# Kernel tuning notes

Measured on AMD Instinct MI355X. Metric: run time of the kernel, lower is better.

The kernel has to match this reference:

```python
import jax, jax.numpy as jnp
import numpy as np
import math

N, E, IN, C, H, ED, B = 50000, 800000, 64, 32, 4, 1, 64
HC = H * C
EPS = 1e-5


def setup_inputs() -> dict:
    key = jax.random.key(0)
    ks = jax.random.split(key, 16)
    def lin(k, fan_in, fan_out):
        s = 1.0 / math.sqrt(fan_in)
        return jax.random.normal(k, (fan_in, fan_out), jnp.float32) * s
    inp = {
        "x": jax.random.normal(ks[0], (N, IN), jnp.float32),
        "edge_index": jax.random.randint(ks[1], (2, E), 0, N, jnp.int64),
        "edge_attr": jax.random.normal(ks[2], (E, ED), jnp.float32),
        "batch_index": jnp.sort(jax.random.randint(ks[3], (N,), 0, B, jnp.int64)),
        # TransformerConv params
        "Wq": lin(ks[4], IN, HC), "bq": jnp.zeros((HC,), jnp.float32),
        "Wk": lin(ks[5], IN, HC), "bk": jnp.zeros((HC,), jnp.float32),
        "Wv": lin(ks[6], IN, HC), "bv": jnp.zeros((HC,), jnp.float32),
        "We": lin(ks[7], ED, HC), "be": jnp.zeros((HC,), jnp.float32),
        "Wskip": lin(ks[8], IN, HC), "bskip": jnp.zeros((HC,), jnp.float32),
        "Wbeta": lin(ks[9], 3 * HC, 1),
        # post linear: H*C -> C
        "Wlin": lin(ks[10], HC, C), "blin": jnp.zeros((C,), jnp.float32),
        # GraphNorm params
        "gn_weight": jnp.ones((C,), jnp.float32),
        "gn_bias": jnp.zeros((C,), jnp.float32),
        "gn_mean_scale": jnp.ones((C,), jnp.float32),
    }
    return inp


def reference(x, edge_index, edge_attr, batch_index, Wq, bq, Wk, bk, Wv, bv,
              We, be, Wskip, bskip, Wbeta, Wlin, blin,
              gn_weight, gn_bias, gn_mean_scale):
    src, dst = edge_index[0], edge_index[1]
    # dense projections [N, H, C]
    q = (x @ Wq + bq).reshape(N, H, C)
    k = (x @ Wk + bk).reshape(N, H, C)
    v = (x @ Wv + bv).reshape(N, H, C)
    e = (edge_attr @ We + be).reshape(E, H, C)
    # per-edge attention logits [E, H]
    k_e = k[src] + e
    alpha = jnp.einsum('ehc,ehc->eh', q[dst], k_e) / math.sqrt(C)
    # segment softmax over incoming edges of each dst node
    m = jax.ops.segment_max(alpha, dst, num_segments=N)  # [N, H]
    a = jnp.exp(alpha - m[dst])
    denom = jax.ops.segment_sum(a, dst, num_segments=N)  # [N, H]
    a = a / jnp.maximum(denom, 1e-16)[dst]
    # (dropout p=0.3 on attention is a no-op in eval mode)
    msg = (v[src] + e) * a[:, :, None]                    # [E, H, C]
    out = jax.ops.segment_sum(msg, dst, num_segments=N).reshape(N, HC)
    # beta-gated skip connection
    x_r = x @ Wskip + bskip                               # [N, HC]
    beta = jax.nn.sigmoid(jnp.concatenate([out, x_r, out - x_r], -1) @ Wbeta)
    out = beta * x_r + (1.0 - beta) * out
    # linear + relu
    h = jax.nn.relu(out @ Wlin + blin)                    # [N, C]
    # GraphNorm over per-graph segments
    ones = jnp.ones((N, 1), h.dtype)
    cnt = jax.ops.segment_sum(ones, batch_index, num_segments=B)  # [B, 1]
    cnt = jnp.maximum(cnt, 1.0)
    mean = jax.ops.segment_sum(h, batch_index, num_segments=B) / cnt
    centered = h - mean[batch_index] * gn_mean_scale
    var = jax.ops.segment_sum(centered * centered, batch_index, num_segments=B) / cnt
    std = jnp.sqrt(var + EPS)
    return gn_weight * centered / std[batch_index] + gn_bias
```

## Files before the change

### kernel.cpp

```cpp
#include <hip/hip_runtime.h>
#include <math.h>

static constexpr int kN  = 50000;
static constexpr int kE  = 800000;
static constexpr int kC  = 32;
static constexpr int kH  = 4;
static constexpr int kHC = 128;
static constexpr int kB  = 64;
static constexpr int kNB = (kN + 255) / 256;
static constexpr int kMB = (kN + 127) / 128;

typedef __attribute__((ext_vector_type(8))) short bf16x8;
typedef __attribute__((ext_vector_type(4))) float f32x4;

__device__ __forceinline__ unsigned short f2bf(float f) {
    unsigned u = __float_as_uint(f);
    unsigned r = (u + 0x7FFFu + ((u >> 16) & 1u)) >> 16;
    return (unsigned short)r;
}
__device__ __forceinline__ float blo(unsigned u) { return __uint_as_float(u << 16); }
__device__ __forceinline__ float bhi(unsigned u) { return __uint_as_float(u & 0xFFFF0000u); }

__global__ __launch_bounds__(256) void hist_packw_kernel(
    const int* __restrict__ ei, int* __restrict__ deg,
    const float* __restrict__ Wq, const float* __restrict__ Wk,
    const float* __restrict__ Wv, const float* __restrict__ Wskip,
    uint4* __restrict__ wtf)
{
    if (blockIdx.x < 16) {
        int tid = blockIdx.x * 256 + threadIdx.x;
        int f = tid >> 6, l = tid & 63;
        int m = f >> 4, c = (f >> 1) & 7, kk = f & 1;
        int col = c * 16 + (l & 15);
        int k0  = kk * 32 + (l >> 4) * 8;
        const float* Wm = (m == 0) ? Wq : (m == 1) ? Wk : (m == 2) ? Wv : Wskip;
        unsigned p[4];
#pragma unroll
        for (int j = 0; j < 4; ++j) {
            unsigned lo = f2bf(Wm[(k0 + 2 * j) * kHC + col]);
            unsigned hi = f2bf(Wm[(k0 + 2 * j + 1) * kHC + col]);
            p[j] = lo | (hi << 16);
        }
        wtf[f * 64 + l] = make_uint4(p[0], p[1], p[2], p[3]);
        return;
    }
    int i = (blockIdx.x - 16) * 256 + threadIdx.x;
    if (i < kE) atomicAdd(&deg[ei[kE + i]], 1);
}

__global__ __launch_bounds__(256) void proj_scanA_kernel(
    const float4* __restrict__ x4,
    const float* __restrict__ bq, const float* __restrict__ bk,
    const float* __restrict__ bv, const float* __restrict__ bskip,
    const uint4* __restrict__ wtf,
    unsigned short* __restrict__ qxb, unsigned short* __restrict__ kvb,
    const int* __restrict__ deg, int* __restrict__ bsum)
{
    __shared__ unsigned stg[2][32 * 128];
    if (blockIdx.x >= kMB) {
        int bid = blockIdx.x - kMB;
        int i = bid * 256 + threadIdx.x;
        int v = (i < kN) ? deg[i] : 0;
#pragma unroll
        for (int s = 1; s < 64; s <<= 1) v += __shfl_xor(v, s);
        if ((threadIdx.x & 63) == 0) stg[0][threadIdx.x >> 6] = (unsigned)v;
        __syncthreads();
        if (threadIdx.x == 0)
            bsum[bid] = (int)(stg[0][0] + stg[0][1] + stg[0][2] + stg[0][3]);
        return;
    }
    const int t = threadIdx.x;
    const int w = t >> 6;
    const int l = t & 63;
    const int l15 = l & 15, l16 = l >> 4;
    const int n0 = blockIdx.x * 128;

    bf16x8 bf[8][2];
#pragma unroll
    for (int c = 0; c < 8; ++c)
#pragma unroll
        for (int kk = 0; kk < 2; ++kk)
            bf[c][kk] = __builtin_bit_cast(bf16x8, wtf[(unsigned)((w * 16 + c * 2 + kk) * 64 + l)]);

    const float* Bm = (w == 0) ? bq : (w == 1) ? bk : (w == 2) ? bv : bskip;
    float bias[8];
#pragma unroll
    for (int c = 0; c < 8; ++c) bias[c] = Bm[c * 16 + l15];

    const int bufid = (w == 0 || w == 3) ? 0 : 1;
    const int add4  = (w >= 2) ? 4 : 0;

    for (int rt = 0; rt < 4; ++rt) {
        const int r0 = n0 + rt * 32 + l15;
        const int r1 = r0 + 16;
        f32x4 acc[2][8];
#pragma unroll
        for (int r = 0; r < 2; ++r)
#pragma unroll
            for (int c = 0; c < 8; ++c)
                acc[r][c] = (f32x4){bias[c], bias[c], bias[c], bias[c]};
#pragma unroll
        for (int kk = 0; kk < 2; ++kk) {
            float4 xa0 = make_float4(0.f,0.f,0.f,0.f), xb0 = xa0, xa1 = xa0, xb1 = xa0;
            if (r0 < kN) {
                xa0 = x4[(size_t)r0 * 16 + kk * 8 + l16 * 2];
                xb0 = x4[(size_t)r0 * 16 + kk * 8 + l16 * 2 + 1];
            }
            if (r1 < kN) {
                xa1 = x4[(size_t)r1 * 16 + kk * 8 + l16 * 2];
                xb1 = x4[(size_t)r1 * 16 + kk * 8 + l16 * 2 + 1];
            }
            uint4 u0 = make_uint4(
                f2bf(xa0.x) | ((unsigned)f2bf(xa0.y) << 16),
                f2bf(xa0.z) | ((unsigned)f2bf(xa0.w) << 16),
                f2bf(xb0.x) | ((unsigned)f2bf(xb0.y) << 16),
                f2bf(xb0.z) | ((unsigned)f2bf(xb0.w) << 16));
            uint4 u1 = make_uint4(
                f2bf(xa1.x) | ((unsigned)f2bf(xa1.y) << 16),
                f2bf(xa1.z) | ((unsigned)f2bf(xa1.w) << 16),
                f2bf(xb1.x) | ((unsigned)f2bf(xb1.y) << 16),
                f2bf(xb1.z) | ((unsigned)f2bf(xb1.w) << 16));
            bf16x8 a0 = __builtin_bit_cast(bf16x8, u0);
            bf16x8 a1 = __builtin_bit_cast(bf16x8, u1);
#pragma unroll
            for (int c = 0; c < 8; ++c) {
                acc[0][c] = __builtin_amdgcn_mfma_f32_16x16x32_bf16(a0, bf[c][kk], acc[0][c], 0, 0, 0);
                acc[1][c] = __builtin_amdgcn_mfma_f32_16x16x32_bf16(a1, bf[c][kk], acc[1][c], 0, 0, 0);
            }
        }
#pragma unroll
        for (int r = 0; r < 2; ++r) {
#pragma unroll
            for (int j = 0; j < 4; ++j) {
                int nn = r * 16 + l16 * 4 + j;
#pragma unroll
                for (int c = 0; c < 8; ++c) {
                    float v0 = acc[r][c][j];
                    float v1 = __shfl_xor(v0, 1);
                    if ((l & 1) == 0) {
                        int jcol = c * 16 + l15;
                        int gpos = ((jcol >> 2) << 3) | (jcol & 3);
                        stg[bufid][nn * 128 + ((gpos + add4) >> 1)] =
                            f2bf(v0) | ((unsigned)f2bf(v1) << 16);
                    }
                }
            }
        }
        __syncthreads();
#pragma unroll
        for (int i = 0; i < 8; ++i) {
            int idx = i * 256 + t;
            int buf = idx >> 10;
            int rem = idx & 1023;
            int nn  = rem >> 5;
            int q4  = rem & 31;
            int node = n0 + rt * 32 + nn;
            if (node < kN)
                ((uint4*)(buf ? kvb : qxb))[(size_t)node * 32 + q4] =
                    *(const uint4*)&stg[buf][nn * 128 + q4 * 4];
        }
        __syncthreads();
    }
}

__global__ __launch_bounds__(256) void scanC2_kernel(
    const int* __restrict__ deg, const int* __restrict__ bsum,
    int* __restrict__ rowptr, int* __restrict__ cursor)
{
    __shared__ int bsh[256];
    __shared__ int sh[256];
    const int t = threadIdx.x, i = blockIdx.x * 256 + t;
    int bv = (t < kNB) ? bsum[t] : 0;
    bsh[t] = bv; __syncthreads();
    for (int off = 1; off < 256; off <<= 1) {
        int u = (t >= off) ? bsh[t - off] : 0;
        __syncthreads();
        bsh[t] += u;
        __syncthreads();
    }
    const int bofs = (blockIdx.x == 0) ? 0 : bsh[blockIdx.x - 1];
    if (blockIdx.x == 0 && t == 0) rowptr[kN] = bsh[kNB - 1];
    int v = (i < kN) ? deg[i] : 0;
    sh[t] = v; __syncthreads();
    for (int off = 1; off < 256; off <<= 1) {
        int u = (t >= off) ? sh[t - off] : 0;
        __syncthreads();
        sh[t] += u;
        __syncthreads();
    }
    if (i < kN) {
        int ex = sh[t] - v + bofs;
        rowptr[i] = ex;
        cursor[i] = ex;
    }
}

__global__ __launch_bounds__(256) void scatter_kernel(
    const int* __restrict__ ei, const float* __restrict__ ea,
    int* __restrict__ cursor, unsigned* __restrict__ csr)
{
    int i = blockIdx.x * 256 + threadIdx.x;
    if (i >= kE) return;
    int dst = ei[kE + i];
    int slot = atomicAdd(&cursor[dst], 1);
    csr[slot] = (unsigned)ei[i] | ((unsigned)f2bf(ea[i]) << 16);
}

__global__ __launch_bounds__(512) void node_attn_kernel(
    const int* __restrict__ rowptr, const unsigned* __restrict__ csr,
    const unsigned short* __restrict__ qxb, const unsigned short* __restrict__ kvb,
    const float* __restrict__ We, const float* __restrict__ be,
    const float* __restrict__ Wbeta, const float* __restrict__ Wlin,
    const float* __restrict__ blin, float* __restrict__ hbuf)
{
    __shared__ float wlS[kHC * kC];
    __shared__ float wbS[3 * kHC];
    __shared__ float oshS[8][kHC];
    const int t = threadIdx.x, wv = t >> 6, lane = t & 63;
    for (int i = t; i < kHC * kC; i += 512) wlS[i] = Wlin[i];
    for (int i = t; i < 3 * kHC; i += 512) wbS[i] = Wbeta[i];
    __syncthreads();

    const int node = blockIdx.x * 8 + wv;
    const int half = lane >> 5;
    const int sl   = lane & 31;
    const int ch   = sl * 4;
    const float4 we4 = *(const float4*)&We[ch];
    const float4 be4 = *(const float4*)&be[ch];
    const float4 wbA = *(const float4*)&wbS[ch];
    const float4 wbB = *(const float4*)&wbS[kHC + ch];
    const float4 wbC = *(const float4*)&wbS[2 * kHC + ch];
    const float blc = blin[sl];
    const float A2 = 0.17677669529663687f * 1.44269504088896341f;

    const uint4 qx = *((const uint4*)(qxb + (size_t)node * 256) + sl);
    const float q0 = blo(qx.x), q1 = bhi(qx.x), q2v = blo(qx.y), q3 = bhi(qx.y);
    const float xr0 = blo(qx.z), xr1 = bhi(qx.z), xr2 = blo(qx.w), xr3 = bhi(qx.w);
    float qw = q0 * we4.x + q1 * we4.y + q2v * we4.z + q3 * we4.w;
    float qe = q0 * be4.x + q1 * be4.y + q2v * be4.z + q3 * be4.w;
    qw += __shfl_xor(qw, 1); qe += __shfl_xor(qe, 1);
    qw += __shfl_xor(qw, 2); qe += __shfl_xor(qe, 2);
    qw += __shfl_xor(qw, 4); qe += __shfl_xor(qe, 4);
    const float qwA = qw * A2, qbA = qe * A2;

    float ss = 0.f, swa = 0.f;
    float ax0 = 0.f, ax1 = 0.f, ax2 = 0.f, ax3 = 0.f;
    const int beg = rowptr[node], end = rowptr[node + 1];
    int e = beg;
    for (; e + 3 < end; e += 4) {
        unsigned cA = csr[e + half];
        unsigned cB = csr[e + 2 + half];
        float aA = bhi(cA), aB = bhi(cB);
        const uint4 uA = *((const uint4*)(kvb + (size_t)(cA & 0xFFFFu) * 256) + sl);
        const uint4 uB = *((const uint4*)(kvb + (size_t)(cB & 0xFFFFu) * 256) + sl);
        float pA = fmaf(q3, bhi(uA.y), fmaf(q2v, blo(uA.y), fmaf(q1, bhi(uA.x), q0 * blo(uA.x))));
        float pB = fmaf(q3, bhi(uB.y), fmaf(q2v, blo(uB.y), fmaf(q1, bhi(uB.x), q0 * blo(uB.x))));
        pA += __shfl_xor(pA, 1); pB += __shfl_xor(pB, 1);
        pA += __shfl_xor(pA, 2); pB += __shfl_xor(pB, 2);
        pA += __shfl_xor(pA, 4); pB += __shfl_xor(pB, 4);
        float eA = __builtin_amdgcn_exp2f(fmaf(pA, A2, fmaf(aA, qwA, qbA)));
        float eB = __builtin_amdgcn_exp2f(fmaf(pB, A2, fmaf(aB, qwA, qbA)));
        ss  += eA + eB;
        swa = fmaf(eA, aA, fmaf(eB, aB, swa));
        ax0 = fmaf(eA, blo(uA.z), fmaf(eB, blo(uB.z), ax0));
        ax1 = fmaf(eA, bhi(uA.z), fmaf(eB, bhi(uB.z), ax1));
        ax2 = fmaf(eA, blo(uA.w), fmaf(eB, blo(uB.w), ax2));
        ax3 = fmaf(eA, bhi(uA.w), fmaf(eB, bhi(uB.w), ax3));
    }
    for (; e < end; e += 2) {
        int idx = e + half;
        bool valid = idx < end;
        unsigned cA = csr[valid ? idx : end - 1];
        float aA = bhi(cA);
        const uint4 uA = *((const uint4*)(kvb + (size_t)(cA & 0xFFFFu) * 256) + sl);
        float pA = fmaf(q3, bhi(uA.y), fmaf(q2v, blo(uA.y), fmaf(q1, bhi(uA.x), q0 * blo(uA.x))));
        pA += __shfl_xor(pA, 1);
        pA += __shfl_xor(pA, 2);
        pA += __shfl_xor(pA, 4);
        float eA = valid ? __builtin_amdgcn_exp2f(fmaf(pA, A2, fmaf(aA, qwA, qbA))) : 0.f;
        ss  += eA;
        swa = fmaf(eA, aA, swa);
        ax0 = fmaf(eA, blo(uA.z), ax0);
        ax1 = fmaf(eA, bhi(uA.z), ax1);
        ax2 = fmaf(eA, blo(uA.w), ax2);
        ax3 = fmaf(eA, bhi(uA.w), ax3);
    }
    ss  += __shfl_xor(ss , 32);
    swa += __shfl_xor(swa, 32);
    ax0 += __shfl_xor(ax0, 32);
    ax1 += __shfl_xor(ax1, 32);
    ax2 += __shfl_xor(ax2, 32);
    ax3 += __shfl_xor(ax3, 32);

    float rcp = 1.f / fmaxf(ss, 1e-16f);
    float v0 = fmaf(swa, we4.x, fmaf(ss, be4.x, ax0)) * rcp;
    float v1 = fmaf(swa, we4.y, fmaf(ss, be4.y, ax1)) * rcp;
    float v2 = fmaf(swa, we4.z, fmaf(ss, be4.z, ax2)) * rcp;
    float v3 = fmaf(swa, we4.w, fmaf(ss, be4.w, ax3)) * rcp;
    float part = wbA.x * v0 + wbA.y * v1 + wbA.z * v2 + wbA.w * v3
               + wbB.x * xr0 + wbB.y * xr1 + wbB.z * xr2 + wbB.w * xr3
               + wbC.x * (v0 - xr0) + wbC.y * (v1 - xr1)
               + wbC.z * (v2 - xr2) + wbC.w * (v3 - xr3);
    part += __shfl_xor(part, 1);
    part += __shfl_xor(part, 2);
    part += __shfl_xor(part, 4);
    part += __shfl_xor(part, 8);
    part += __shfl_xor(part, 16);
    float beta = 1.f / (1.f + __expf(-part));
    float o0 = beta * xr0 + (1.f - beta) * v0;
    float o1 = beta * xr1 + (1.f - beta) * v1;
    float o2 = beta * xr2 + (1.f - beta) * v2;
    float o3 = beta * xr3 + (1.f - beta) * v3;
    if (half == 0) *(float4*)&oshS[wv][ch] = make_float4(o0, o1, o2, o3);
    __builtin_amdgcn_wave_barrier();
    float hp = 0.f;
#pragma unroll
    for (int jj = 0; jj < 64; ++jj) {
        int j = half * 64 + jj;
        hp = fmaf(oshS[wv][j], wlS[j * kC + sl], hp);
    }
    hp += __shfl_xor(hp, 32);
    if (lane < 32) hbuf[(size_t)node * kC + sl] = fmaxf(hp + blc, 0.f);
}

__global__ __launch_bounds__(256) void gn_reduce_kernel(
    const float* __restrict__ hbuf, const int* __restrict__ batch,
    const float* __restrict__ gms, float* __restrict__ stats)
{
    const int g = blockIdx.x;
    const int t = threadIdx.x;
    __shared__ int se[2];
    __shared__ float s1[8][kC], s2[8][kC];
    if (t < 2) {
        int target = g + t;
        int lo = 0, hi = kN;
        while (lo < hi) { int mid = (lo + hi) >> 1; if (batch[mid] < target) lo = mid + 1; else hi = mid; }
        se[t] = lo;
    }
    __syncthreads();
    int start = se[0], end = se[1];
    float cnt = fmaxf((float)(end - start), 1.f);
    int c = t & 31, r = t >> 5;
    float a = 0.f, b = 0.f;
    for (int n = start + r; n < end; n += 8) {
        float v = hbuf[(size_t)n * kC + c];
        a += v; b = fmaf(v, v, b);
    }
    s1[r][c] = a; s2[r][c] = b;
    __syncthreads();
    if (t < kC) {
        float sa = 0.f, sb = 0.f;
#pragma unroll
        for (int i = 0; i < 8; ++i) { sa += s1[i][t]; sb += s2[i][t]; }
        float mean = sa / cnt;
        float ms   = mean * gms[t];
        float var  = sb / cnt - 2.f * ms * mean + ms * ms;
        stats[g * 64 + t]      = ms;
        stats[g * 64 + 32 + t] = rsqrtf(var + 1e-5f);
    }
}

__global__ __launch_bounds__(256) void gn_apply_kernel(
    const float* __restrict__ hbuf, const int* __restrict__ batch,
    const float* __restrict__ stats,
    const float* __restrict__ gw, const float* __restrict__ gb,
    float* __restrict__ out)
{
    int idx = blockIdx.x * 256 + threadIdx.x;
    if (idx >= kN * kC) return;
    int n = idx >> 5, c = idx & 31;
    int g = batch[n];
    float ms   = stats[g * 64 + c];
    float rstd = stats[g * 64 + 32 + c];
    float v = hbuf[idx];
    out[idx] = fmaf(gw[c] * (v - ms), rstd, gb[c]);
}

extern "C" void kernel_launch(void* const* d_in, const int* in_sizes, int n_in,
                              void* d_out, int out_size, void* d_ws, size_t ws_size,
                              hipStream_t stream) {
    (void)in_sizes; (void)n_in; (void)out_size; (void)ws_size;
    const float* x     = (const float*)d_in[0];
    const int*   ei    = (const int*)d_in[1];
    const float* ea    = (const float*)d_in[2];
    const int*   batch = (const int*)d_in[3];
    const float* Wq    = (const float*)d_in[4];
    const float* bq    = (const float*)d_in[5];
    const float* Wk    = (const float*)d_in[6];
    const float* bk    = (const float*)d_in[7];
    const float* Wv    = (const float*)d_in[8];
    const float* bv    = (const float*)d_in[9];
    const float* We    = (const float*)d_in[10];
    const float* be    = (const float*)d_in[11];
    const float* Wskip = (const float*)d_in[12];
    const float* bskip = (const float*)d_in[13];
    const float* Wbeta = (const float*)d_in[14];
    const float* Wlin  = (const float*)d_in[15];
    const float* blin  = (const float*)d_in[16];
    const float* gw    = (const float*)d_in[17];
    const float* gb    = (const float*)d_in[18];
    const float* gms   = (const float*)d_in[19];
    float* out = (float*)d_out;

    char* ws = (char*)d_ws;
    unsigned* csr = (unsigned*)ws;        ws += (size_t)kE * 4;
    unsigned short* qxb = (unsigned short*)ws; ws += (size_t)kN * 256 * 2;
    unsigned short* kvb = (unsigned short*)ws; ws += (size_t)kN * 256 * 2;
    float* hbuf   = (float*)ws;           ws += (size_t)kN * kC * 4;
    int*   deg    = (int*)ws;             ws += (size_t)kN * 4;
    int*   cursor = (int*)ws;             ws += (size_t)kN * 4;
    int*   rowptr = (int*)ws;             ws += (size_t)(kN + 1) * 4;
    int*   bsum   = (int*)ws;             ws += (size_t)kNB * 4;
    float* stats  = (float*)ws;           ws += (size_t)kB * 64 * 4;
    uint4* wtf    = (uint4*)ws;           ws += (size_t)64 * 64 * 16;

    hipMemsetAsync(deg, 0, (size_t)kN * 4, stream);

    hist_packw_kernel<<<16 + (kE + 255) / 256, 256, 0, stream>>>(
        ei, deg, Wq, Wk, Wv, Wskip, wtf);
    proj_scanA_kernel<<<kMB + kNB, 256, 0, stream>>>(
        (const float4*)x, bq, bk, bv, bskip, wtf, qxb, kvb, deg, bsum);
    scanC2_kernel<<<kNB, 256, 0, stream>>>(deg, bsum, rowptr, cursor);
    scatter_kernel<<<(kE + 255) / 256, 256, 0, stream>>>(ei, ea, cursor, csr);
    node_attn_kernel<<<kN / 8, 512, 0, stream>>>(
        rowptr, csr, qxb, kvb, We, be, Wbeta, Wlin, blin, hbuf);
    gn_reduce_kernel<<<kB, 256, 0, stream>>>(hbuf, batch, gms, stats);
    gn_apply_kernel<<<(kN * kC + 255) / 256, 256, 0, stream>>>(
        hbuf, batch, stats, gw, gb, out);
}
```

Measured before the change: 238.7 us.

## Fuse GraphNorm reduce and apply; drop LDS staging in projection stores

The GraphNorm statistics and normalization passes are merged into one kernel with 512 threads per graph segment. Each block computes its segment's mean and rstd, keeps them in shared memory, and then normalizes the same rows, which removes a launch and the global stats buffer. Separately, the projection kernel now writes packed bf16 results straight to global memory instead of staging them in 32KB of LDS and copying out with uint4 stores. This drops two barriers per tile and frees LDS for occupancy, at the cost of scattered 4-byte writes from half the lanes. The fused GN kernel uses only 64 blocks, so its second pass over hbuf may be less parallel than the old grid-wide apply kernel.

```diff
diff --git a/kernel.cpp b/kernel.cpp
--- a/kernel.cpp
+++ b/kernel.cpp
@@ -56,17 +56,16 @@
     unsigned short* __restrict__ qxb, unsigned short* __restrict__ kvb,
     const int* __restrict__ deg, int* __restrict__ bsum)
 {
-    __shared__ unsigned stg[2][32 * 128];
+    __shared__ int sh4[4];
     if (blockIdx.x >= kMB) {
         int bid = blockIdx.x - kMB;
         int i = bid * 256 + threadIdx.x;
         int v = (i < kN) ? deg[i] : 0;
 #pragma unroll
         for (int s = 1; s < 64; s <<= 1) v += __shfl_xor(v, s);
-        if ((threadIdx.x & 63) == 0) stg[0][threadIdx.x >> 6] = (unsigned)v;
+        if ((threadIdx.x & 63) == 0) sh4[threadIdx.x >> 6] = v;
         __syncthreads();
-        if (threadIdx.x == 0)
-            bsum[bid] = (int)(stg[0][0] + stg[0][1] + stg[0][2] + stg[0][3]);
+        if (threadIdx.x == 0) bsum[bid] = sh4[0] + sh4[1] + sh4[2] + sh4[3];
         return;
     }
     const int t = threadIdx.x;
@@ -87,8 +86,8 @@
 #pragma unroll
     for (int c = 0; c < 8; ++c) bias[c] = Bm[c * 16 + l15];
 
-    const int bufid = (w == 0 || w == 3) ? 0 : 1;
-    const int add4  = (w >= 2) ? 4 : 0;
+    unsigned short* dst = (w == 0 || w == 3) ? qxb : kvb;
+    const int add4 = (w >= 2) ? 4 : 0;
 
     for (int rt = 0; rt < 4; ++rt) {
         const int r0 = n0 + rt * 32 + l15;
@@ -132,34 +131,22 @@
         for (int r = 0; r < 2; ++r) {
 #pragma unroll
             for (int j = 0; j < 4; ++j) {
-                int nn = r * 16 + l16 * 4 + j;
+                int node = n0 + rt * 32 + r * 16 + l16 * 4 + j;
+                bool valid = (node < kN) && ((l & 1) == 0);
+                size_t base = (size_t)node * 128;
 #pragma unroll
                 for (int c = 0; c < 8; ++c) {
                     float v0 = acc[r][c][j];
                     float v1 = __shfl_xor(v0, 1);
-                    if ((l & 1) == 0) {
+                    if (valid) {
                         int jcol = c * 16 + l15;
                         int gpos = ((jcol >> 2) << 3) | (jcol & 3);
-                        stg[bufid][nn * 128 + ((gpos + add4) >> 1)] =
-                            f2bf(v0) | ((unsigned)f2bf(v1) << 16);
+                        unsigned pk = f2bf(v0) | ((unsigned)f2bf(v1) << 16);
+                        ((unsigned*)dst)[base + ((gpos + add4) >> 1)] = pk;
                     }
                 }
             }
         }
-        __syncthreads();
-#pragma unroll
-        for (int i = 0; i < 8; ++i) {
-            int idx = i * 256 + t;
-            int buf = idx >> 10;
-            int rem = idx & 1023;
-            int nn  = rem >> 5;
-            int q4  = rem & 31;
-            int node = n0 + rt * 32 + nn;
-            if (node < kN)
-                ((uint4*)(buf ? kvb : qxb))[(size_t)node * 32 + q4] =
-                    *(const uint4*)&stg[buf][nn * 128 + q4 * 4];
-        }
-        __syncthreads();
     }
 }
 
@@ -323,14 +310,17 @@
     if (lane < 32) hbuf[(size_t)node * kC + sl] = fmaxf(hp + blc, 0.f);
 }
 
-__global__ __launch_bounds__(256) void gn_reduce_kernel(
+__global__ __launch_bounds__(512) void gn_kernel(
     const float* __restrict__ hbuf, const int* __restrict__ batch,
-    const float* __restrict__ gms, float* __restrict__ stats)
+    const float* __restrict__ gms,
+    const float* __restrict__ gw, const float* __restrict__ gb,
+    float* __restrict__ out)
 {
     const int g = blockIdx.x;
     const int t = threadIdx.x;
     __shared__ int se[2];
-    __shared__ float s1[8][kC], s2[8][kC];
+    __shared__ float s1[16][kC], s2[16][kC];
+    __shared__ float msS[kC], rsS[kC];
     if (t < 2) {
         int target = g + t;
         int lo = 0, hi = kN;
@@ -342,7 +332,7 @@
     float cnt = fmaxf((float)(end - start), 1.f);
     int c = t & 31, r = t >> 5;
     float a = 0.f, b = 0.f;
-    for (int n = start + r; n < end; n += 8) {
+    for (int n = start + r; n < end; n += 16) {
         float v = hbuf[(size_t)n * kC + c];
         a += v; b = fmaf(v, v, b);
     }
@@ -351,29 +341,19 @@
     if (t < kC) {
         float sa = 0.f, sb = 0.f;
 #pragma unroll
-        for (int i = 0; i < 8; ++i) { sa += s1[i][t]; sb += s2[i][t]; }
+        for (int i = 0; i < 16; ++i) { sa += s1[i][t]; sb += s2[i][t]; }
         float mean = sa / cnt;
         float ms   = mean * gms[t];
         float var  = sb / cnt - 2.f * ms * mean + ms * ms;
-        stats[g * 64 + t]      = ms;
-        stats[g * 64 + 32 + t] = rsqrtf(var + 1e-5f);
-    }
-}
-
-__global__ __launch_bounds__(256) void gn_apply_kernel(
-    const float* __restrict__ hbuf, const int* __restrict__ batch,
-    const float* __restrict__ stats,
-    const float* __restrict__ gw, const float* __restrict__ gb,
-    float* __restrict__ out)
-{
-    int idx = blockIdx.x * 256 + threadIdx.x;
-    if (idx >= kN * kC) return;
-    int n = idx >> 5, c = idx & 31;
-    int g = batch[n];
-    float ms   = stats[g * 64 + c];
-    float rstd = stats[g * 64 + 32 + c];
-    float v = hbuf[idx];
-    out[idx] = fmaf(gw[c] * (v - ms), rstd, gb[c]);
+        msS[t] = ms;
+        rsS[t] = rsqrtf(var + 1e-5f);
+    }
+    __syncthreads();
+    float ms = msS[c], rs = rsS[c], w = gw[c], bb = gb[c];
+    for (int n = start + r; n < end; n += 16) {
+        float v = hbuf[(size_t)n * kC + c];
+        out[(size_t)n * kC + c] = fmaf(w * (v - ms), rs, bb);
+    }
 }
 
 extern "C" void kernel_launch(void* const* d_in, const int* in_sizes, int n_in,
@@ -411,7 +391,6 @@
     int*   cursor = (int*)ws;             ws += (size_t)kN * 4;
     int*   rowptr = (int*)ws;             ws += (size_t)(kN + 1) * 4;
     int*   bsum   = (int*)ws;             ws += (size_t)kNB * 4;
-    float* stats  = (float*)ws;           ws += (size_t)kB * 64 * 4;
     uint4* wtf    = (uint4*)ws;           ws += (size_t)64 * 64 * 16;
 
     hipMemsetAsync(deg, 0, (size_t)kN * 4, stream);
@@ -424,7 +403,5 @@
     scatter_kernel<<<(kE + 255) / 256, 256, 0, stream>>>(ei, ea, cursor, csr);
     node_attn_kernel<<<kN / 8, 512, 0, stream>>>(
         rowptr, csr, qxb, kvb, We, be, Wbeta, Wlin, blin, hbuf);
-    gn_reduce_kernel<<<kB, 256, 0, stream>>>(hbuf, batch, gms, stats);
-    gn_apply_kernel<<<(kN * kC + 255) / 256, 256, 0, stream>>>(
-        hbuf, batch, stats, gw, gb, out);
-}
+    gn_kernel<<<kB, 512, 0, stream>>>(hbuf, batch, gms, gw, gb, out);
+}
```

Result: faster. 220.3 us (median of 2 runs) (-7.7%).
